# Performance work log

Hardware: AMD Instinct MI355X
Metric: run time of the kernel (lower is better)

## Reference

```python
import jax, jax.numpy as jnp
import numpy as np

B, CIN, COUT, L = 16, 128, 128, 4096  # kernel_size == L required by the broadcast in the source
STRIDE, DIL, PAD = 1, 1, 0


def setup_inputs() -> dict:
    key = jax.random.key(0)
    kx, kw, kb = jax.random.split(key, 3)
    x = jax.random.normal(kx, (B, CIN, L), dtype=jnp.float32)
    # source does weight.data.int() then .float() in forward -> integer-truncated randn
    weight = jnp.trunc(jax.random.normal(kw, (COUT, CIN, L), dtype=jnp.float32))
    bias = jax.random.normal(kb, (COUT,), dtype=jnp.float32)
    return {"x": x, "weight": weight, "bias": bias}


def reference(x, weight, bias):
    # padding=0 -> F.pad is a no-op; output_size = (L + 2*0 - 1*(K-1) - 1)//1 + 1 = 1
    out_size = (L + 2 * PAD - DIL * (L - 1) - 1) // STRIDE + 1  # == 1
    x_f = jnp.fft.fft(x, axis=2)            # [B, Cin, L] complex64
    w_f = jnp.fft.fft(weight, axis=2)       # [Cout, Cin, L] complex64
    # faithful math of (x_f[:,None] * w_f[None]).sum(dim=2), expressed as a
    # per-frequency complex contraction to avoid the O(B*Cout*Cin*L) intermediate
    out_f = jnp.einsum('bil,oil->bol', x_f, w_f)  # [B, Cout, L]
    out = jnp.fft.ifft(out_f, axis=2).real
    out = out + bias[None, :, None]
    return out[:, :, :out_size]
```

## Files before the change

kernel.cpp:

```cpp
#include <hip/hip_runtime.h>


constexpr int LEN   = 4096;
constexpr int CIN_  = 128;
constexpr int COUT_ = 128;
constexpr int BATCH = 16;

__global__ void init_out_kernel(const float* __restrict__ bias, float* __restrict__ out) {
    int t = blockIdx.x * 256 + threadIdx.x;
    if (t < BATCH * COUT_) out[t] = bias[t & (COUT_ - 1)];
}

__global__ __launch_bounds__(256, 2)
void conv_fft_dot_kernel(const float* __restrict__ x, const float* __restrict__ w,
                         float* __restrict__ out) {
    __shared__ float lds[17408];

    const int tid   = threadIdx.x;
    const int lane  = tid & 63;
    const int wv    = tid >> 6;
    const int bk    = blockIdx.x;
    const int ot    = bk >> 6;
    const int kg    = bk & 63;
    const int obase = ot * 16 + wv * 4;

    float acc[16][4];
#pragma unroll
    for (int b = 0; b < 16; ++b)
#pragma unroll
        for (int j = 0; j < 4; ++j) acc[b][j] = 0.f;

    for (int q = 0; q < 8; ++q) {
        const int kc = kg * 8 + q;
        const int ci = kc >> 2;
        const int m0 = (kc & 3) << 10;

        __syncthreads();
        {
            const int nbase = LEN - m0 - tid;
#pragma unroll
            for (int b = 0; b < 16; ++b) {
                const float* xp = x + ((b * CIN_ + ci) << 12);
                float* lp = lds + (b << 10) + tid;
#pragma unroll
                for (int p = 0; p < 4; ++p) {
                    int n = (nbase - (p << 8)) & (LEN - 1);
                    lp[p << 8] = xp[n];
                }
            }
        }
        __syncthreads();

        const float4* wp0 = (const float4*)(w + (((obase + 0) * CIN_ + ci) << 12) + m0);
        const float4* wp1 = (const float4*)(w + (((obase + 1) * CIN_ + ci) << 12) + m0);
        const float4* wp2 = (const float4*)(w + (((obase + 2) * CIN_ + ci) << 12) + m0);
        const float4* wp3 = (const float4*)(w + (((obase + 3) * CIN_ + ci) << 12) + m0);

        float4 wr[4];
        wr[0] = wp0[lane]; wr[1] = wp1[lane]; wr[2] = wp2[lane]; wr[3] = wp3[lane];
#pragma unroll
        for (int s = 0; s < 4; ++s) {
            float4 wn[4];
            if (s < 3) {
                const int off = (s + 1) * 64 + lane;
                wn[0] = wp0[off]; wn[1] = wp1[off]; wn[2] = wp2[off]; wn[3] = wp3[off];
            }
            const float4* xls = (const float4*)lds + s * 64 + lane;
#pragma unroll
            for (int b = 0; b < 16; ++b) {
                float4 xv = xls[b << 8];
#pragma unroll
                for (int j = 0; j < 4; ++j) {
                    acc[b][j] += xv.x * wr[j].x;
                    acc[b][j] += xv.y * wr[j].y;
                    acc[b][j] += xv.z * wr[j].z;
                    acc[b][j] += xv.w * wr[j].w;
                }
            }
            if (s < 3) { wr[0] = wn[0]; wr[1] = wn[1]; wr[2] = wn[2]; wr[3] = wn[3]; }
        }
    }

    __syncthreads();
#pragma unroll
    for (int b = 0; b < 16; ++b)
#pragma unroll
        for (int j = 0; j < 4; ++j)
            lds[(wv * 64 + b * 4 + j) * 68 + lane] = acc[b][j];
    __syncthreads();
    {
        const int wv2 = tid >> 6, st = tid & 63;
        const float4* row = (const float4*)(lds + (wv2 * 64 + st) * 68);
        float sum = 0.f;
#pragma unroll
        for (int l = 0; l < 16; ++l) {
            float4 v = row[l];
            sum += v.x + v.y + v.z + v.w;
        }
        const int b = st >> 2, j = st & 3;
        const int o = ot * 16 + wv2 * 4 + j;
        atomicAdd(out + b * COUT_ + o, sum);
    }
}

extern "C" void kernel_launch(void* const* d_in, const int* in_sizes, int n_in,
                              void* d_out, int out_size, void* d_ws, size_t ws_size,
                              hipStream_t stream) {
    const float* x    = (const float*)d_in[0];
    const float* wgt  = (const float*)d_in[1];
    const float* bias = (const float*)d_in[2];
    float* out = (float*)d_out;
    (void)in_sizes; (void)n_in; (void)d_ws; (void)ws_size; (void)out_size;

    init_out_kernel<<<8, 256, 0, stream>>>(bias, out);
    conv_fft_dot_kernel<<<512, 256, 0, stream>>>(x, wgt, out);
}
```

Baseline: 396.7 us.

## Double-buffer x staging via global_load_lds and widen per-wave output tile

Each block now owns one input channel and 32 output channels, with 8 outputs per wave instead of 4. This doubles reuse of every x value read from LDS. The reversed x slices are staged straight into a double-buffered LDS area with global_load_lds, so the next chunk's load overlaps compute on the current one and there is one barrier per iteration. The cost is more accumulator registers (128 floats) plus the weight registers, which risks spills or lower occupancy, and the reduction is split into two passes.

Result: slower. 535.2 us (+34.9%).

```diff
diff --git a/kernel.cpp b/kernel.cpp
--- a/kernel.cpp
+++ b/kernel.cpp
@@ -11,6 +11,27 @@
     if (t < BATCH * COUT_) out[t] = bias[t & (COUT_ - 1)];
 }
 
+__device__ __forceinline__ void gload_lds4(const float* g, float* l) {
+    __builtin_amdgcn_global_load_lds(
+        (const __attribute__((address_space(1))) unsigned int*)g,
+        (__attribute__((address_space(3))) unsigned int*)l, 4, 0, 0);
+}
+
+__device__ __forceinline__ void stage_chunk(const float* __restrict__ x, float* dst_base,
+                                            int ci, int m0, int wv, int lane) {
+#pragma unroll
+    for (int bb = 0; bb < 4; ++bb) {
+        const int b = 4 * wv + bb;
+        const float* xc = x + ((b * CIN_ + ci) << 12);
+        float* dstb = dst_base + (b << 9);
+#pragma unroll
+        for (int t = 0; t < 8; ++t) {
+            const int n = (LEN - m0 - (t << 6) - lane) & (LEN - 1);
+            gload_lds4(xc + n, dstb + (t << 6));
+        }
+    }
+}
+
 __global__ __launch_bounds__(256, 2)
 void conv_fft_dot_kernel(const float* __restrict__ x, const float* __restrict__ w,
                          float* __restrict__ out) {
@@ -18,88 +39,84 @@
 
     const int tid   = threadIdx.x;
     const int lane  = tid & 63;
-    const int wv    = tid >> 6;
+    const int wv    = __builtin_amdgcn_readfirstlane(tid >> 6);
     const int bk    = blockIdx.x;
-    const int ot    = bk >> 6;
-    const int kg    = bk & 63;
-    const int obase = ot * 16 + wv * 4;
+    const int ot    = bk >> 7;
+    const int ci    = bk & 127;
+    const int obase = ot * 32 + wv * 8;
 
-    float acc[16][4];
+    float acc[16][8];
 #pragma unroll
     for (int b = 0; b < 16; ++b)
 #pragma unroll
-        for (int j = 0; j < 4; ++j) acc[b][j] = 0.f;
+        for (int j = 0; j < 8; ++j) acc[b][j] = 0.f;
 
+    stage_chunk(x, lds, ci, 0, wv, lane);
+    __syncthreads();
+
+#pragma unroll 1
     for (int q = 0; q < 8; ++q) {
-        const int kc = kg * 8 + q;
-        const int ci = kc >> 2;
-        const int m0 = (kc & 3) << 10;
+        const int m0 = q << 9;
+        const float4* __restrict__ xb = (const float4*)(lds + ((q & 1) << 13));
 
-        __syncthreads();
-        {
-            const int nbase = LEN - m0 - tid;
+        float4 w0[8], w1[8];
 #pragma unroll
-            for (int b = 0; b < 16; ++b) {
-                const float* xp = x + ((b * CIN_ + ci) << 12);
-                float* lp = lds + (b << 10) + tid;
+        for (int j = 0; j < 8; ++j) {
+            const float4* wp = (const float4*)(w + (((obase + j) * CIN_ + ci) << 12) + m0);
+            w0[j] = wp[lane];
+            w1[j] = wp[64 + lane];
+        }
+
+        if (q < 7)
+            stage_chunk(x, lds + (((q + 1) & 1) << 13), ci, (q + 1) << 9, wv, lane);
+
 #pragma unroll
-                for (int p = 0; p < 4; ++p) {
-                    int n = (nbase - (p << 8)) & (LEN - 1);
-                    lp[p << 8] = xp[n];
-                }
+        for (int b = 0; b < 16; ++b) {
+            const float4 xv = xb[(b << 7) + lane];
+#pragma unroll
+            for (int j = 0; j < 8; ++j) {
+                acc[b][j] += xv.x * w0[j].x;
+                acc[b][j] += xv.y * w0[j].y;
+                acc[b][j] += xv.z * w0[j].z;
+                acc[b][j] += xv.w * w0[j].w;
+            }
+        }
+#pragma unroll
+        for (int b = 0; b < 16; ++b) {
+            const float4 xv = xb[(b << 7) + 64 + lane];
+#pragma unroll
+            for (int j = 0; j < 8; ++j) {
+                acc[b][j] += xv.x * w1[j].x;
+                acc[b][j] += xv.y * w1[j].y;
+                acc[b][j] += xv.z * w1[j].z;
+                acc[b][j] += xv.w * w1[j].w;
             }
         }
         __syncthreads();
-
-        const float4* wp0 = (const float4*)(w + (((obase + 0) * CIN_ + ci) << 12) + m0);
-        const float4* wp1 = (const float4*)(w + (((obase + 1) * CIN_ + ci) << 12) + m0);
-        const float4* wp2 = (const float4*)(w + (((obase + 2) * CIN_ + ci) << 12) + m0);
-        const float4* wp3 = (const float4*)(w + (((obase + 3) * CIN_ + ci) << 12) + m0);
-
-        float4 wr[4];
-        wr[0] = wp0[lane]; wr[1] = wp1[lane]; wr[2] = wp2[lane]; wr[3] = wp3[lane];
-#pragma unroll
-        for (int s = 0; s < 4; ++s) {
-            float4 wn[4];
-            if (s < 3) {
-                const int off = (s + 1) * 64 + lane;
-                wn[0] = wp0[off]; wn[1] = wp1[off]; wn[2] = wp2[off]; wn[3] = wp3[off];
-            }
-            const float4* xls = (const float4*)lds + s * 64 + lane;
-#pragma unroll
-            for (int b = 0; b < 16; ++b) {
-                float4 xv = xls[b << 8];
-#pragma unroll
-                for (int j = 0; j < 4; ++j) {
-                    acc[b][j] += xv.x * wr[j].x;
-                    acc[b][j] += xv.y * wr[j].y;
-                    acc[b][j] += xv.z * wr[j].z;
-                    acc[b][j] += xv.w * wr[j].w;
-                }
-            }
-            if (s < 3) { wr[0] = wn[0]; wr[1] = wn[1]; wr[2] = wn[2]; wr[3] = wn[3]; }
-        }
     }
 
-    __syncthreads();
+#pragma unroll 1
+    for (int pass = 0; pass < 2; ++pass) {
+        if (pass) __syncthreads();
 #pragma unroll
-    for (int b = 0; b < 16; ++b)
+        for (int b = 0; b < 16; ++b)
 #pragma unroll
-        for (int j = 0; j < 4; ++j)
-            lds[(wv * 64 + b * 4 + j) * 68 + lane] = acc[b][j];
-    __syncthreads();
-    {
-        const int wv2 = tid >> 6, st = tid & 63;
-        const float4* row = (const float4*)(lds + (wv2 * 64 + st) * 68);
-        float sum = 0.f;
+            for (int jj = 0; jj < 4; ++jj)
+                lds[(wv * 64 + b * 4 + jj) * 68 + lane] = acc[b][pass * 4 + jj];
+        __syncthreads();
+        {
+            const int st = tid & 63;
+            const float4* row = (const float4*)(lds + (wv * 64 + st) * 68);
+            float sum = 0.f;
 #pragma unroll
-        for (int l = 0; l < 16; ++l) {
-            float4 v = row[l];
-            sum += v.x + v.y + v.z + v.w;
+            for (int l = 0; l < 16; ++l) {
+                const float4 v = row[l];
+                sum += v.x + v.y + v.z + v.w;
+            }
+            const int b = st >> 2, jj = st & 3;
+            const int o = obase + pass * 4 + jj;
+            atomicAdd(out + b * COUT_ + o, sum);
         }
-        const int b = st >> 2, j = st & 3;
-        const int o = ot * 16 + wv2 * 4 + j;
-        atomicAdd(out + b * COUT_ + o, sum);
     }
 }
 
```
